# Kernel tuning notes

Hardware: AMD Instinct MI355X
Metric: run time of the kernel (lower is better)

The kernel has to match this reference:

```python
import jax, jax.numpy as jnp
import numpy as np

B, N, NS, C, H = 2, 2048, 2048, 512, 8
HD = C // H
SCALE = HD ** -0.5
NEG = -10000.0


def setup_inputs() -> dict:
    key = jax.random.key(0)
    ks = jax.random.split(key, 9)
    q = jax.random.normal(ks[0], (B, N, C), dtype=jnp.float32)
    k = jax.random.normal(ks[1], (B, NS, C), dtype=jnp.float32)
    v = jax.random.normal(ks[2], (B, NS, C), dtype=jnp.float32)
    # 1.0 marks invalid support positions (gets -10000 added)
    supp_valid_mask = (jax.random.uniform(ks[3], (B, NS)) < 0.2).astype(jnp.float32)
    # binary fg/bg support mask used for cycle consistency
    supp_mask = jax.random.randint(ks[4], (B, NS), 0, 2, dtype=jnp.int32)
    w = 0.02
    Wq = jax.random.normal(ks[5], (C, C), dtype=jnp.float32) * w
    Wk = jax.random.normal(ks[6], (C, C), dtype=jnp.float32) * w
    Wv = jax.random.normal(ks[7], (C, C), dtype=jnp.float32) * w
    Wproj = jax.random.normal(ks[8], (C, C), dtype=jnp.float32) * w
    return {"q": q, "k": k, "v": v, "supp_valid_mask": supp_valid_mask,
            "supp_mask": supp_mask, "Wq": Wq, "Wk": Wk, "Wv": Wv, "Wproj": Wproj}


def reference(q, k, v, supp_valid_mask, supp_mask, Wq, Wk, Wv, Wproj):
    b, n, c = q.shape
    ns = k.shape[1]
    # linear projections (torch Linear: x @ W^T), split heads -> [B,H,N,HD]
    qh = (q @ Wq.T).reshape(b, n, H, HD).transpose(0, 2, 1, 3)
    kh = (k @ Wk.T).reshape(b, ns, H, HD).transpose(0, 2, 1, 3)
    vh = (v @ Wv.T).reshape(b, ns, H, HD).transpose(0, 2, 1, 3)
    attn = jnp.einsum('bhnd,bhmd->bhnm', qh, kh) * SCALE  # [B,H,N,NS]

    # cycle-consistency association (vectorized over heads)
    k2q = jnp.argmax(attn, axis=2)                    # [B,H,NS] idx into N
    q2k = jnp.argmax(attn, axis=3)                    # [B,H,N]  idx into NS
    re_map_idx = jnp.take_along_axis(q2k, k2q, axis=2)  # [B,H,NS]
    sm = jnp.broadcast_to(supp_mask[:, None, :], (b, H, ns))
    re_map_mask = jnp.take_along_axis(sm, re_map_idx, axis=2)
    asso = sm == re_map_mask                          # [B,H,NS] bool

    # mark cycle-inconsistent positions invalid (eval: ass_drop is identity)
    valid = jnp.broadcast_to(supp_valid_mask[:, None, :], (b, H, ns))
    valid = jnp.where(asso, valid, 1.0)

    attn = attn + (valid * NEG)[:, :, None, :]
    attn = jax.nn.softmax(attn, axis=-1)
    x = jnp.einsum('bhnm,bhmd->bhnd', attn, vh)       # [B,H,N,HD]
    x = x.transpose(0, 2, 1, 3).reshape(b, n, c)
    return x @ Wproj.T
```

## Files before the change

### kernel.cpp

```cpp
#include <hip/hip_runtime.h>
#include <hip/hip_bf16.h>
#include <stdint.h>

#define H_ 8
#define NS_ 2048
#define C_ 512
#define HD_ 64
#define SCALE_ 0.125f
#define NEG_ -10000.0f
#define LOG2E_ 1.4426950408889634f
#define MFIX_ 4.0f

typedef _Float16 f16x8_t __attribute__((ext_vector_type(8)));
typedef _Float16 f16x4_t __attribute__((ext_vector_type(4)));
typedef float f32x4_t __attribute__((ext_vector_type(4)));

#define MFMAH(a, b, c) __builtin_amdgcn_mfma_f32_16x16x32_f16(a, b, c, 0, 0, 0)

__device__ inline f16x8_t load_h8(const _Float16* p) {
    return *reinterpret_cast<const f16x8_t*>(p);
}

__device__ inline void gload_lds16(const void* g, void* l) {
    __builtin_amdgcn_global_load_lds(
        (const __attribute__((address_space(1))) unsigned int*)g,
        (__attribute__((address_space(3))) unsigned int*)l, 16, 0, 0);
}

__device__ inline unsigned orderF(float v) {
    unsigned u = __float_as_uint(v);
    return (u & 0x80000000u) ? ~u : (u | 0x80000000u);
}
__device__ inline unsigned long long packVR(float v, int idx) {
    return ((unsigned long long)orderF(v) << 32) | (unsigned)(~idx);
}
__device__ inline unsigned long long max64(unsigned long long a, unsigned long long b) {
    return a > b ? a : b;
}
__device__ inline unsigned long long shflx64(unsigned long long x, int m) {
    unsigned lo = (unsigned)x, hi = (unsigned)(x >> 32);
    lo = __shfl_xor(lo, m, 64);
    hi = __shfl_xor(hi, m, 64);
    return ((unsigned long long)hi << 32) | lo;
}

__global__ __launch_bounds__(256) void wsplit4(
        const float* __restrict__ w0, const float* __restrict__ w1,
        const float* __restrict__ w2, const float* __restrict__ w3,
        _Float16* __restrict__ hi, _Float16* __restrict__ lo)
{
    const int i = blockIdx.x * 256 + threadIdx.x;
    const int y = blockIdx.y;
    const float* src = (y == 0) ? w0 : (y == 1) ? w1 : (y == 2) ? w2 : w3;
    const float4 v = reinterpret_cast<const float4*>(src)[i];
    f16x4_t hv, lv;
    hv[0] = (_Float16)v.x; hv[1] = (_Float16)v.y;
    hv[2] = (_Float16)v.z; hv[3] = (_Float16)v.w;
    lv[0] = (_Float16)(v.x - (float)hv[0]);
    lv[1] = (_Float16)(v.y - (float)hv[1]);
    lv[2] = (_Float16)(v.z - (float)hv[2]);
    lv[3] = (_Float16)(v.w - (float)hv[3]);
    const size_t o = ((size_t)y << 16) + i;
    reinterpret_cast<f16x4_t*>(hi)[o] = hv;
    reinterpret_cast<f16x4_t*>(lo)[o] = lv;
}

__global__ __launch_bounds__(256) void proj_gemm(
        const float* __restrict__ qin, const float* __restrict__ kin,
        const float* __restrict__ vin,
        const _Float16* __restrict__ wHall, const _Float16* __restrict__ wLall,
        _Float16* __restrict__ qhi, _Float16* __restrict__ qlo,
        _Float16* __restrict__ khi, _Float16* __restrict__ klo,
        _Float16* __restrict__ vT)
{
    __shared__ __attribute__((aligned(16))) _Float16 Wsh[2][2][4096];
    const int zz = blockIdx.z;
    const float* A32 = (zz == 0) ? qin : (zz == 1) ? kin : vin;
    const _Float16* Wh = wHall + ((size_t)zz << 18);
    const _Float16* Wl = wLall + ((size_t)zz << 18);
    const int t = threadIdx.x, w = t >> 6, lane = t & 63;
    const int m16 = lane & 15, quad = lane >> 4;
    const int bm = blockIdx.x << 7, bn = blockIdx.y << 6;
    const int r0 = bm + (w << 5) + m16, r1 = r0 + 16;
    const int krow = lane >> 3, kblk = (lane & 7) ^ (krow & 7);
    const int e = m16 & 7;
    const int s00 = (quad ^ e) << 3, s01 = ((4 + quad) ^ e) << 3;
    const f32x4_t z = {0.f, 0.f, 0.f, 0.f};
    f32x4_t acc[2][4];
    #pragma unroll
    for (int rs = 0; rs < 2; rs++)
        #pragma unroll
        for (int tl = 0; tl < 4; tl++) acc[rs][tl] = z;

    auto stageW = [&](int buf, int kc) {
        #pragma unroll
        for (int ci = 0; ci < 4; ci++) {
            const int pp = (w << 2) + ci;
            const int s = pp >> 3, pj = pp & 7;
            const _Float16* src = (s ? Wl : Wh)
                + (size_t)(bn + (pj << 3) + krow) * C_ + kc + (kblk << 3);
            gload_lds16(src, &Wsh[buf][s][pj << 9]);
        }
    };
    auto loadA = [&](int kc, f16x8_t* d) {
        #pragma unroll
        for (int rs = 0; rs < 2; rs++) {
            const float* pr = A32 + (size_t)(rs ? r1 : r0) * C_ + kc + (quad << 3);
            #pragma unroll
            for (int seg = 0; seg < 2; seg++) {
                f16x8_t hv, lv;
                #pragma unroll
                for (int i = 0; i < 8; i++) {
                    const float x = pr[seg * 32 + i];
                    const _Float16 hh = (_Float16)x;
                    hv[i] = hh;
                    lv[i] = (_Float16)(x - (float)hh);
                }
                d[rs * 4 + seg] = hv;
                d[rs * 4 + seg + 2] = lv;
            }
        }
    };

    f16x8_t cA[8], nA[8];
    stageW(0, 0);
    loadA(0, cA);
    for (int ch = 0; ch < 8; ch++) {
        __syncthreads();
        if (ch + 1 < 8) {
            stageW((ch + 1) & 1, (ch + 1) << 6);
            loadA((ch + 1) << 6, nA);
        }
        const _Float16* W0 = Wsh[ch & 1][0];
        const _Float16* W1 = Wsh[ch & 1][1];
        #pragma unroll
        for (int tl = 0; tl < 4; tl++) {
            const int j64 = ((tl << 4) + m16) << 6;
            const f16x8_t bh0 = load_h8(&W0[j64 + s00]);
            const f16x8_t bh1 = load_h8(&W0[j64 + s01]);
            const f16x8_t bl0 = load_h8(&W1[j64 + s00]);
            const f16x8_t bl1 = load_h8(&W1[j64 + s01]);
            f32x4_t c0 = acc[0][tl];
            c0 = MFMAH(cA[0], bh0, c0); c0 = MFMAH(cA[1], bh1, c0);
            c0 = MFMAH(cA[2], bh0, c0); c0 = MFMAH(cA[3], bh1, c0);
            c0 = MFMAH(cA[0], bl0, c0); c0 = MFMAH(cA[1], bl1, c0);
            acc[0][tl] = c0;
            f32x4_t c1 = acc[1][tl];
            c1 = MFMAH(cA[4], bh0, c1); c1 = MFMAH(cA[5], bh1, c1);
            c1 = MFMAH(cA[6], bh0, c1); c1 = MFMAH(cA[7], bh1, c1);
            c1 = MFMAH(cA[4], bl0, c1); c1 = MFMAH(cA[5], bl1, c1);
            acc[1][tl] = c1;
        }
        #pragma unroll
        for (int i = 0; i < 8; i++) cA[i] = nA[i];
    }
    const int by = blockIdx.y;
    _Float16* o1 = (zz == 0) ? qhi : khi;
    _Float16* o2 = (zz == 0) ? qlo : klo;
    #pragma unroll
    for (int rs = 0; rs < 2; rs++) {
        #pragma unroll
        for (int tl = 0; tl < 4; tl++) {
            #pragma unroll
            for (int r = 0; r < 4; r++) {
                const int gr = bm + (w << 5) + (rs << 4) + (quad << 2) + r;
                const float val = acc[rs][tl][r];
                const int b = gr >> 11, n = gr & 2047;
                const int d = (tl << 4) + m16;
                const int bh = (b << 3) + by;
                if (zz == 2) {
                    const int kp = ((n & 15) << 1) | ((n >> 4) & 1);
                    vT[(((size_t)((bh << 6) + (n >> 5)) << 6) + d) * 32 + kp] = (_Float16)val;
                } else {
                    const size_t idx = ((((size_t)bh << 11) + n) << 6) + d;
                    const _Float16 hh = (_Float16)val;
                    o1[idx] = hh;
                    o2[idx] = (_Float16)(val - (float)hh);
                }
            }
        }
    }
}

__global__ __launch_bounds__(256) void argmax_mfma(
        const _Float16* __restrict__ qhi, const _Float16* __restrict__ qlo,
        const _Float16* __restrict__ khi, const _Float16* __restrict__ klo,
        unsigned long long* __restrict__ rowP, unsigned long long* __restrict__ colP)
{
    __shared__ __attribute__((aligned(16))) _Float16 Ksh[2][2][4096];
    __shared__ unsigned long long colbest[512];
    const int bx = blockIdx.x;
    const int bh = ((bx & 7) << 1) | (bx >> 9);
    const int mid = (bx >> 3) & 63;
    const int rt = mid & 15;
    const int ks = mid >> 4;
    const int t = threadIdx.x, w = t >> 6, lane = t & 63;
    const int m16 = lane & 15, quad = lane >> 4;
    const int wrow = (rt << 7) + (w << 5);
    const size_t qoff0 = ((((size_t)bh << 11) + wrow + m16) << 6) + (quad << 3);
    const size_t qoff1 = qoff0 + 1024;
    const f16x8_t a00h = load_h8(qhi + qoff0), a01h = load_h8(qhi + qoff0 + 32);
    const f16x8_t a00l = load_h8(qlo + qoff0), a01l = load_h8(qlo + qoff0 + 32);
    const f16x8_t a10h = load_h8(qhi + qoff1), a11h = load_h8(qhi + qoff1 + 32);
    const f16x8_t a10l = load_h8(qlo + qoff1), a11l = load_h8(qlo + qoff1 + 32);
    for (int c = t; c < 512; c += 256) colbest[c] = 0;
    const int krow = lane >> 3, kblk = (lane & 7) ^ (krow & 7);
    const int e = m16 & 7;
    const int s00 = (quad ^ e) << 3, s01 = ((4 + quad) ^ e) << 3;
    const size_t kbase = (((size_t)bh << 11) + (ks << 9)) << 6;
    float bv0[4] = {-3.4e38f, -3.4e38f, -3.4e38f, -3.4e38f};
    float bv1[4] = {-3.4e38f, -3.4e38f, -3.4e38f, -3.4e38f};
    int bc0[4] = {0, 0, 0, 0}, bc1[4] = {0, 0, 0, 0};
    const f32x4_t z = {0.f, 0.f, 0.f, 0.f};

    auto stage = [&](int buf, int cidx) {
        const size_t ce = kbase + ((size_t)cidx << 12);
        #pragma unroll
        for (int ci = 0; ci < 4; ci++) {
            const int pp = (w << 2) + ci;
            const int s = pp >> 3, pj = pp & 7;
            const _Float16* src = (s ? klo : khi) + ce + (((pj << 3) + krow) << 6) + (kblk << 3);
            gload_lds16(src, &Ksh[buf][s][pj << 9]);
        }
    };

    stage(0, 0);
    for (int ch = 0; ch < 8; ch++) {
        __syncthreads();
        if (ch + 1 < 8) stage((ch + 1) & 1, ch + 1);
        const _Float16* K0 = Ksh[ch & 1][0];
        const _Float16* K1 = Ksh[ch & 1][1];
        const int kc0 = (ks << 9) + (ch << 6);
        #pragma unroll
        for (int tl = 0; tl < 4; tl++) {
            const int j64 = ((tl << 4) + m16) << 6;
            const f16x8_t bh0 = load_h8(&K0[j64 + s00]);
            const f16x8_t bh1 = load_h8(&K0[j64 + s01]);
            const f16x8_t bl0 = load_h8(&K1[j64 + s00]);
            const f16x8_t bl1 = load_h8(&K1[j64 + s01]);
            f32x4_t c0 = MFMAH(a00h, bh0, z);
            c0 = MFMAH(a01h, bh1, c0);
            c0 = MFMAH(a00l, bh0, c0); c0 = MFMAH(a01l, bh1, c0);
            c0 = MFMAH(a00h, bl0, c0); c0 = MFMAH(a01h, bl1, c0);
            f32x4_t c1 = MFMAH(a10h, bh0, z);
            c1 = MFMAH(a11h, bh1, c1);
            c1 = MFMAH(a10l, bh0, c1); c1 = MFMAH(a11l, bh1, c1);
            c1 = MFMAH(a10h, bl0, c1); c1 = MFMAH(a11h, bl1, c1);
            const int gc = kc0 + (tl << 4) + m16;
            #pragma unroll
            for (int r = 0; r < 4; r++) {
                if (c0[r] > bv0[r]) { bv0[r] = c0[r]; bc0[r] = gc; }
                if (c1[r] > bv1[r]) { bv1[r] = c1[r]; bc1[r] = gc; }
            }
            float v = c0[0]; int ri = (quad << 2);
            if (c0[1] > v) { v = c0[1]; ri = (quad << 2) + 1; }
            if (c0[2] > v) { v = c0[2]; ri = (quad << 2) + 2; }
            if (c0[3] > v) { v = c0[3]; ri = (quad << 2) + 3; }
            if (c1[0] > v) { v = c1[0]; ri = 16 + (quad << 2); }
            if (c1[1] > v) { v = c1[1]; ri = 16 + (quad << 2) + 1; }
            if (c1[2] > v) { v = c1[2]; ri = 16 + (quad << 2) + 2; }
            if (c1[3] > v) { v = c1[3]; ri = 16 + (quad << 2) + 3; }
            unsigned long long pk = packVR(v, wrow + ri);
            pk = max64(pk, shflx64(pk, 16));
            pk = max64(pk, shflx64(pk, 32));
            if (quad == 0) atomicMax(&colbest[(ch << 6) + (tl << 4) + m16], pk);
        }
    }
    #pragma unroll
    for (int r = 0; r < 4; r++) {
        unsigned long long p0 = packVR(bv0[r], bc0[r]);
        p0 = max64(p0, shflx64(p0, 1)); p0 = max64(p0, shflx64(p0, 2));
        p0 = max64(p0, shflx64(p0, 4)); p0 = max64(p0, shflx64(p0, 8));
        if (m16 == 0)
            atomicMax(rowP + ((size_t)bh << 11) + wrow + (quad << 2) + r, p0);
        unsigned long long p1 = packVR(bv1[r], bc1[r]);
        p1 = max64(p1, shflx64(p1, 1)); p1 = max64(p1, shflx64(p1, 2));
        p1 = max64(p1, shflx64(p1, 4)); p1 = max64(p1, shflx64(p1, 8));
        if (m16 == 0)
            atomicMax(rowP + ((size_t)bh << 11) + wrow + 16 + (quad << 2) + r, p1);
    }
    __syncthreads();
    for (int c = t; c < 512; c += 256)
        atomicMax(colP + ((size_t)bh << 11) + (ks << 9) + c, colbest[c]);
}

__global__ __launch_bounds__(256) void resolve(const unsigned long long* __restrict__ q2kP,
        const unsigned long long* __restrict__ k2qP, const int* __restrict__ supp_mask,
        const float* __restrict__ supp_valid, float* __restrict__ vn)
{
    const int t = blockIdx.x * 256 + threadIdx.x;
    const int bh = t >> 11, j = t & 2047, b = bh >> 3;
    const unsigned k2q = 0xFFFFFFFFu - (unsigned)(k2qP[t] & 0xFFFFFFFFull);
    const unsigned rm  = 0xFFFFFFFFu - (unsigned)(q2kP[(bh << 11) + k2q] & 0xFFFFFFFFull);
    const int asso = supp_mask[(b << 11) + j] == supp_mask[(b << 11) + (int)rm];
    const float valid = asso ? supp_valid[(b << 11) + j] : 1.0f;
    vn[t] = fmaf(valid, NEG_ * LOG2E_, -MFIX_);
}

__global__ __launch_bounds__(256) void attn_pv(
        const _Float16* __restrict__ qh, const _Float16* __restrict__ kh,
        const _Float16* __restrict__ vT, const float* __restrict__ vnG,
        float* __restrict__ xp, float* __restrict__ lp)
{
    __shared__ __attribute__((aligned(16))) _Float16 Ksh[2][2048];
    __shared__ __attribute__((aligned(16))) _Float16 Vsh[2][2048];
    __shared__ float vnL[1024];
    __shared__ __attribute__((aligned(16))) unsigned pbuf[4][320];
    const int bx = blockIdx.x;
    const int bh = ((bx & 7) << 1) | (bx >> 9);
    const int mid = (bx >> 3) & 63;
    const int rt = mid & 31, ks = mid >> 5;
    const int t = threadIdx.x, w = t >> 6, lane = t & 63;
    const int m16 = lane & 15, quad = lane >> 4;
    const int rowbase = (rt << 6) + (w << 4);
    const size_t qoff = ((((size_t)bh << 11) + rowbase + m16) << 6) + (quad << 3);
    const f16x8_t a0 = load_h8(qh + qoff), a1 = load_h8(qh + qoff + 32);
    for (int c = t; c < 1024; c += 256) vnL[c] = vnG[(bh << 11) + (ks << 10) + c];
    const float KS = SCALE_ * LOG2E_;
    const int krow = lane >> 3, kblk = (lane & 7) ^ ((lane >> 3) & 7);
    const int vrow = lane >> 2, vblk = (lane & 3) ^ ((lane >> 3) & 3);
    const int e = m16 & 7;
    const int s00 = (quad ^ e) << 3, s01 = ((4 + quad) ^ e) << 3;
    const int vsw = (m16 >> 1) & 3;
    f16x8_t ones;
    #pragma unroll
    for (int i = 0; i < 8; i++) ones[i] = (_Float16)1.0f;
    const f32x4_t z = {0.f, 0.f, 0.f, 0.f};
    f32x4_t xacc[4];
    #pragma unroll
    for (int nt = 0; nt < 4; nt++) xacc[nt] = z;
    f32x4_t lacc = z;
    const size_t kbel = ((size_t)bh << 11) * HD_;
    unsigned* pw = pbuf[w];

    auto stage = [&](int buf, int ch) {
        const int kcg = (ks << 10) + (ch << 5);
        const size_t ce = kbel + (size_t)kcg * HD_;
        const size_t ve = ((size_t)(bh << 6) + (kcg >> 5)) << 11;
        #pragma unroll
        for (int ci = 0; ci < 2; ci++) {
            const int call = (w << 1) + ci;
            if (call < 4) {
                const _Float16* src = kh + ce + ((call * 8 + krow) << 6) + (kblk << 3);
                gload_lds16(src, &Ksh[buf][call << 9]);
            } else {
                const int j = call - 4;
                const _Float16* src = vT + ve + ((j * 16 + vrow) << 5) + (vblk << 3);
                gload_lds16(src, &Vsh[buf][j << 9]);
            }
        }
    };

    stage(0, 0);
    for (int ch = 0; ch < 32; ch++) {
        __syncthreads();
        if (ch + 1 < 32) stage((ch + 1) & 1, ch + 1);
        const _Float16* K = Ksh[ch & 1];
        const _Float16* V = Vsh[ch & 1];
        const f16x8_t b00 = load_h8(&K[(m16 << 6) + s00]);
        const f16x8_t b01 = load_h8(&K[(m16 << 6) + s01]);
        const f16x8_t b10 = load_h8(&K[((16 + m16) << 6) + s00]);
        const f16x8_t b11 = load_h8(&K[((16 + m16) << 6) + s01]);
        f32x4_t c0 = MFMAH(a0, b00, z); c0 = MFMAH(a1, b01, c0);
        f32x4_t c1 = MFMAH(a0, b10, z); c1 = MFMAH(a1, b11, c1);
        const float vn0 = vnL[(ch << 5) + m16], vn1 = vnL[(ch << 5) + 16 + m16];
        #pragma unroll
        for (int r = 0; r < 4; r++) {
            const float p0 = exp2f(fmaf(c0[r], KS, vn0));
            const float p1 = exp2f(fmaf(c1[r], KS, vn1));
            union { _Float16 h[2]; unsigned u; } pk_;
            pk_.h[0] = (_Float16)p0;
            pk_.h[1] = (_Float16)p1;
            pw[((quad << 2) + r) * 20 + m16] = pk_.u;
        }
        __threadfence_block();
        const f16x8_t pa = *reinterpret_cast<const f16x8_t*>(&pw[m16 * 20 + (quad << 2)]);
        lacc = MFMAH(pa, ones, lacc);
        #pragma unroll
        for (int nt = 0; nt < 4; nt++) {
            const f16x8_t vb = load_h8(&V[((nt * 16 + m16) << 5) + ((quad ^ vsw) << 3)]);
            xacc[nt] = MFMAH(pa, vb, xacc[nt]);
        }
    }
    const int b = bh >> 3, h = bh & 7;
    if (m16 == 0) {
        #pragma unroll
        for (int r = 0; r < 4; r++)
            lp[((size_t)ks << 15) + (bh << 11) + rowbase + (quad << 2) + r] = lacc[r];
    }
    const size_t xbase = ((size_t)ks << 21);
    #pragma unroll
    for (int r = 0; r < 4; r++) {
        const int row = rowbase + (quad << 2) + r;
        #pragma unroll
        for (int nt = 0; nt < 4; nt++)
            xp[xbase + (((size_t)(b << 11) + row) << 9) + (h << 6) + (nt << 4) + m16] = xacc[nt][r];
    }
}

__global__ __launch_bounds__(256) void out_gemm(
        const float* __restrict__ xp, const float* __restrict__ lp,
        const _Float16* __restrict__ Wh, const _Float16* __restrict__ Wl,
        float* __restrict__ outF)
{
    __shared__ __attribute__((aligned(16))) _Float16 Wsh[2][2][4096];
    const int t = threadIdx.x, w = t >> 6, lane = t & 63;
    const int m16 = lane & 15, quad = lane >> 4;
    const int bm = blockIdx.x << 7, bn = blockIdx.y << 6;
    const int r0 = bm + (w << 5) + m16, r1 = r0 + 16;
    const int krow = lane >> 3, kblk = (lane & 7) ^ (krow & 7);
    const int e = m16 & 7;
    const int s00 = (quad ^ e) << 3, s01 = ((4 + quad) ^ e) << 3;
    const f32x4_t z = {0.f, 0.f, 0.f, 0.f};
    f32x4_t acc[2][4];
    #pragma unroll
    for (int rs = 0; rs < 2; rs++)
        #pragma unroll
        for (int tl = 0; tl < 4; tl++) acc[rs][tl] = z;

    auto stageW = [&](int buf, int kc) {
        #pragma unroll
        for (int ci = 0; ci < 4; ci++) {
            const int pp = (w << 2) + ci;
            const int s = pp >> 3, pj = pp & 7;
            const _Float16* src = (s ? Wl : Wh)
                + (size_t)(bn + (pj << 3) + krow) * C_ + kc + (kblk << 3);
            gload_lds16(src, &Wsh[buf][s][pj << 9]);
        }
    };
    auto loadA = [&](int ch, f16x8_t* d) {
        const int kc = ch << 6;
        #pragma unroll
        for (int rs = 0; rs < 2; rs++) {
            const int r = rs ? r1 : r0;
            const int b = r >> 11, n = r & 2047;
            const size_t li = ((size_t)((b << 3) + ch) << 11) + n;
            const float linv = 1.0f / (lp[li] + lp[32768 + li]);
            const size_t base = ((size_t)r << 9) + kc + (quad << 3);
            #pragma unroll
            for (int seg = 0; seg < 2; seg++) {
                f16x8_t hv, lv;
                #pragma unroll
                for (int i = 0; i < 8; i++) {
                    const size_t o = base + seg * 32 + i;
                    const float x = (xp[o] + xp[2097152 + o]) * linv;
                    const _Float16 hh = (_Float16)x;
                    hv[i] = hh;
                    lv[i] = (_Float16)(x - (float)hh);
                }
                d[rs * 4 + seg] = hv;
                d[rs * 4 + seg + 2] = lv;
            }
        }
    };

    f16x8_t cA[8], nA[8];
    stageW(0, 0);
    loadA(0, cA);
    for (int ch = 0; ch < 8; ch++) {
        __syncthreads();
        if (ch + 1 < 8) {
            stageW((ch + 1) & 1, (ch + 1) << 6);
            loadA(ch + 1, nA);
        }
        const _Float16* W0 = Wsh[ch & 1][0];
        const _Float16* W1 = Wsh[ch & 1][1];
        #pragma unroll
        for (int tl = 0; tl < 4; tl++) {
            const int j64 = ((tl << 4) + m16) << 6;
            const f16x8_t bh0 = load_h8(&W0[j64 + s00]);
            const f16x8_t bh1 = load_h8(&W0[j64 + s01]);
            const f16x8_t bl0 = load_h8(&W1[j64 + s00]);
            const f16x8_t bl1 = load_h8(&W1[j64 + s01]);
            f32x4_t c0 = acc[0][tl];
            c0 = MFMAH(cA[0], bh0, c0); c0 = MFMAH(cA[1], bh1, c0);
            c0 = MFMAH(cA[2], bh0, c0); c0 = MFMAH(cA[3], bh1, c0);
            c0 = MFMAH(cA[0], bl0, c0); c0 = MFMAH(cA[1], bl1, c0);
            acc[0][tl] = c0;
            f32x4_t c1 = acc[1][tl];
            c1 = MFMAH(cA[4], bh0, c1); c1 = MFMAH(cA[5], bh1, c1);
            c1 = MFMAH(cA[6], bh0, c1); c1 = MFMAH(cA[7], bh1, c1);
            c1 = MFMAH(cA[4], bl0, c1); c1 = MFMAH(cA[5], bl1, c1);
            acc[1][tl] = c1;
        }
        #pragma unroll
        for (int i = 0; i < 8; i++) cA[i] = nA[i];
    }
    #pragma unroll
    for (int rs = 0; rs < 2; rs++) {
        #pragma unroll
        for (int tl = 0; tl < 4; tl++) {
            #pragma unroll
            for (int r = 0; r < 4; r++) {
                const int gr = bm + (w << 5) + (rs << 4) + (quad << 2) + r;
                const int gj = bn + (tl << 4) + m16;
                outF[(size_t)gr * C_ + gj] = acc[rs][tl][r];
            }
        }
    }
}

extern "C" void kernel_launch(void* const* d_in, const int* in_sizes, int n_in,
                              void* d_out, int out_size, void* d_ws, size_t ws_size,
                              hipStream_t stream) {
    const float* q  = (const float*)d_in[0];
    const float* k  = (const float*)d_in[1];
    const float* v  = (const float*)d_in[2];
    const float* supp_valid = (const float*)d_in[3];
    const int*   supp_mask  = (const int*)d_in[4];
    const float* Wq = (const float*)d_in[5];
    const float* Wk = (const float*)d_in[6];
    const float* Wv = (const float*)d_in[7];
    const float* Wp = (const float*)d_in[8];
    float* out = (float*)d_out;

    char* p = (char*)d_ws;
    _Float16* qhi = (_Float16*)p;      p += 4194304;
    _Float16* qlo = (_Float16*)p;      p += 4194304;
    _Float16* khi = (_Float16*)p;      p += 4194304;
    _Float16* klo = (_Float16*)p;      p += 4194304;
    _Float16* vT  = (_Float16*)p;      p += 4194304;
    float* xp     = (float*)p;         p += 16777216;
    _Float16* wH  = (_Float16*)p;      p += 2097152;
    _Float16* wL  = (_Float16*)p;      p += 2097152;
    unsigned long long* q2kP = (unsigned long long*)p; p += 262144;
    unsigned long long* k2qP = (unsigned long long*)p; p += 262144;
    float* lp = (float*)p;             p += 262144;
    float* validNeg = (float*)p;       p += 131072;

    hipMemsetAsync(q2kP, 0, 524288, stream);

    dim3 bG(256);
    wsplit4<<<dim3(256, 4), bG, 0, stream>>>(Wq, Wk, Wv, Wp, wH, wL);
    proj_gemm<<<dim3(32, 8, 3), bG, 0, stream>>>(q, k, v, wH, wL,
                                                 qhi, qlo, khi, klo, vT);

    argmax_mfma<<<1024, bG, 0, stream>>>(qhi, qlo, khi, klo, q2kP, k2qP);

    resolve<<<128, bG, 0, stream>>>(q2kP, k2qP, supp_mask, supp_valid, validNeg);

    attn_pv<<<1024, bG, 0, stream>>>(qhi, khi, vT, validNeg, xp, lp);

    out_gemm<<<dim3(32, 8), bG, 0, stream>>>(xp, lp,
                                             wH + 3 * 262144, wL + 3 * 262144, out);
}
```

Measured before the change: 220.6 us.

## Keep softmax probabilities in registers by transposing the QK MFMA and repacking V

The QK^T MFMA operands are swapped so each lane's score outputs already match the A-operand layout that the PV MFMA expects. This removes the per-chunk LDS round trip through pbuf along with its fence. The V transpose layout in the projection kernel is permuted to match the new probability ordering. The change also uses the raw exp2 and packed round-toward-zero f16 conversion intrinsics, loads the mask bias as a vector, and precomputes the staging pointers. It risks mismatched k-ordering between P and V if the permutation is wrong, and the conversion now rounds toward zero.

New measurement: 214.8 us. -2.6%, faster.

```diff
diff --git a/kernel.cpp b/kernel.cpp
--- a/kernel.cpp
+++ b/kernel.cpp
@@ -13,6 +13,7 @@
 
 typedef _Float16 f16x8_t __attribute__((ext_vector_type(8)));
 typedef _Float16 f16x4_t __attribute__((ext_vector_type(4)));
+typedef __fp16 h16x2_t __attribute__((ext_vector_type(2)));
 typedef float f32x4_t __attribute__((ext_vector_type(4)));
 
 #define MFMAH(a, b, c) __builtin_amdgcn_mfma_f32_16x16x32_f16(a, b, c, 0, 0, 0)
@@ -169,7 +170,7 @@
                 const int d = (tl << 4) + m16;
                 const int bh = (b << 3) + by;
                 if (zz == 2) {
-                    const int kp = ((n & 15) << 1) | ((n >> 4) & 1);
+                    const int kp = (((n >> 2) & 3) << 3) | (((n >> 4) & 1) << 2) | (n & 3);
                     vT[(((size_t)((bh << 6) + (n >> 5)) << 6) + d) * 32 + kp] = (_Float16)val;
                 } else {
                     const size_t idx = ((((size_t)bh << 11) + n) << 6) + d;
@@ -304,8 +305,7 @@
 {
     __shared__ __attribute__((aligned(16))) _Float16 Ksh[2][2048];
     __shared__ __attribute__((aligned(16))) _Float16 Vsh[2][2048];
-    __shared__ float vnL[1024];
-    __shared__ __attribute__((aligned(16))) unsigned pbuf[4][320];
+    __shared__ __attribute__((aligned(16))) float vnL[1024];
     const int bx = blockIdx.x;
     const int bh = ((bx & 7) << 1) | (bx >> 9);
     const int mid = (bx >> 3) & 63;
@@ -330,51 +330,60 @@
     #pragma unroll
     for (int nt = 0; nt < 4; nt++) xacc[nt] = z;
     f32x4_t lacc = z;
+
     const size_t kbel = ((size_t)bh << 11) * HD_;
-    unsigned* pw = pbuf[w];
-
-    auto stage = [&](int buf, int ch) {
-        const int kcg = (ks << 10) + (ch << 5);
-        const size_t ce = kbel + (size_t)kcg * HD_;
-        const size_t ve = ((size_t)(bh << 6) + (kcg >> 5)) << 11;
-        #pragma unroll
-        for (int ci = 0; ci < 2; ci++) {
-            const int call = (w << 1) + ci;
-            if (call < 4) {
-                const _Float16* src = kh + ce + ((call * 8 + krow) << 6) + (kblk << 3);
-                gload_lds16(src, &Ksh[buf][call << 9]);
-            } else {
-                const int j = call - 4;
-                const _Float16* src = vT + ve + ((j * 16 + vrow) << 5) + (vblk << 3);
-                gload_lds16(src, &Vsh[buf][j << 9]);
-            }
-        }
+    const bool isK = (w < 2);
+    const _Float16* src0;
+    const _Float16* src1;
+    _Float16* dst0a; _Float16* dst0b; _Float16* dst1a; _Float16* dst1b;
+    if (isK) {
+        const int call0 = w << 1;
+        src0 = kh + kbel + ((size_t)ks << 16) + (((call0 << 3) + krow) << 6) + (kblk << 3);
+        src1 = src0 + 512;
+        dst0a = &Ksh[0][call0 << 9]; dst0b = &Ksh[1][call0 << 9];
+        dst1a = &Ksh[0][(call0 + 1) << 9]; dst1b = &Ksh[1][(call0 + 1) << 9];
+    } else {
+        const int j0 = (w - 2) << 1;
+        src0 = vT + (((size_t)(bh << 6) + (ks << 5)) << 11)
+                  + (((j0 << 4) + vrow) << 5) + (vblk << 3);
+        src1 = src0 + 512;
+        dst0a = &Vsh[0][j0 << 9]; dst0b = &Vsh[1][j0 << 9];
+        dst1a = &Vsh[0][(j0 + 1) << 9]; dst1b = &Vsh[1][(j0 + 1) << 9];
+    }
+    auto stage = [&](int buf) {
+        gload_lds16(src0, buf ? dst0b : dst0a);
+        gload_lds16(src1, buf ? dst1b : dst1a);
+        src0 += 2048; src1 += 2048;
     };
 
-    stage(0, 0);
+    stage(0);
     for (int ch = 0; ch < 32; ch++) {
         __syncthreads();
-        if (ch + 1 < 32) stage((ch + 1) & 1, ch + 1);
+        if (ch + 1 < 32) stage((ch + 1) & 1);
         const _Float16* K = Ksh[ch & 1];
         const _Float16* V = Vsh[ch & 1];
         const f16x8_t b00 = load_h8(&K[(m16 << 6) + s00]);
         const f16x8_t b01 = load_h8(&K[(m16 << 6) + s01]);
         const f16x8_t b10 = load_h8(&K[((16 + m16) << 6) + s00]);
         const f16x8_t b11 = load_h8(&K[((16 + m16) << 6) + s01]);
-        f32x4_t c0 = MFMAH(a0, b00, z); c0 = MFMAH(a1, b01, c0);
-        f32x4_t c1 = MFMAH(a0, b10, z); c1 = MFMAH(a1, b11, c1);
-        const float vn0 = vnL[(ch << 5) + m16], vn1 = vnL[(ch << 5) + 16 + m16];
-        #pragma unroll
-        for (int r = 0; r < 4; r++) {
-            const float p0 = exp2f(fmaf(c0[r], KS, vn0));
-            const float p1 = exp2f(fmaf(c1[r], KS, vn1));
-            union { _Float16 h[2]; unsigned u; } pk_;
-            pk_.h[0] = (_Float16)p0;
-            pk_.h[1] = (_Float16)p1;
-            pw[((quad << 2) + r) * 20 + m16] = pk_.u;
-        }
-        __threadfence_block();
-        const f16x8_t pa = *reinterpret_cast<const f16x8_t*>(&pw[m16 * 20 + (quad << 2)]);
+        f32x4_t c0 = MFMAH(b00, a0, z); c0 = MFMAH(b01, a1, c0);
+        f32x4_t c1 = MFMAH(b10, a0, z); c1 = MFMAH(b11, a1, c1);
+        const f32x4_t vn0 = *reinterpret_cast<const f32x4_t*>(&vnL[(ch << 5) + (quad << 2)]);
+        const f32x4_t vn1 = *reinterpret_cast<const f32x4_t*>(&vnL[(ch << 5) + 16 + (quad << 2)]);
+        union { h16x2_t h2[4]; f16x8_t v8; } pk;
+        pk.h2[0] = __builtin_amdgcn_cvt_pkrtz(
+            __builtin_amdgcn_exp2f(fmaf(c0[0], KS, vn0[0])),
+            __builtin_amdgcn_exp2f(fmaf(c0[1], KS, vn0[1])));
+        pk.h2[1] = __builtin_amdgcn_cvt_pkrtz(
+            __builtin_amdgcn_exp2f(fmaf(c0[2], KS, vn0[2])),
+            __builtin_amdgcn_exp2f(fmaf(c0[3], KS, vn0[3])));
+        pk.h2[2] = __builtin_amdgcn_cvt_pkrtz(
+            __builtin_amdgcn_exp2f(fmaf(c1[0], KS, vn1[0])),
+            __builtin_amdgcn_exp2f(fmaf(c1[1], KS, vn1[1])));
+        pk.h2[3] = __builtin_amdgcn_cvt_pkrtz(
+            __builtin_amdgcn_exp2f(fmaf(c1[2], KS, vn1[2])),
+            __builtin_amdgcn_exp2f(fmaf(c1[3], KS, vn1[3])));
+        const f16x8_t pa = pk.v8;
         lacc = MFMAH(pa, ones, lacc);
         #pragma unroll
         for (int nt = 0; nt < 4; nt++) {
@@ -528,7 +537,7 @@
     float* lp = (float*)p;             p += 262144;
     float* validNeg = (float*)p;       p += 131072;
 
-    hipMemsetAsync(q2kP, 0, 524288, stream);
+    (void)hipMemsetAsync(q2kP, 0, 524288, stream);
 
     dim3 bG(256);
     wsplit4<<<dim3(256, 4), bG, 0, stream>>>(Wq, Wk, Wv, Wp, wH, wL);
```
